# Performance work log

Hardware: AMD Instinct MI355X
Metric: run time of the kernel (lower is better)

## Reference

```python
import jax, jax.numpy as jnp
import numpy as np

DIM = 1024
HEADS = 8
DIM_HEAD = 64
INNER = HEADS * DIM_HEAD  # 512
LN_EPS = 1e-5


def setup_inputs() -> dict:
    key = jax.random.key(0)
    ks = jax.random.split(key, 8)
    b, n, m = 4, 2048, 512
    x = jax.random.normal(ks[0], (b, n, DIM), dtype=jnp.float32)
    media = jax.random.normal(ks[1], (b, m, DIM), dtype=jnp.float32)
    media_mask = jax.random.randint(ks[2], (b, m), 0, 2).astype(jnp.bool_)
    media_mask = media_mask.at[:, 0].set(True)  # avoid fully-masked rows
    ln_g = jnp.ones((DIM,), jnp.float32)
    ln_b = jnp.zeros((DIM,), jnp.float32)
    s = 0.02
    Wq = jax.random.normal(ks[3], (DIM, INNER), jnp.float32) * s
    Wkv = jax.random.normal(ks[4], (DIM, 2 * INNER), jnp.float32) * s
    Wo = jax.random.normal(ks[5], (INNER, DIM), jnp.float32) * s
    return {"x": x, "media": media, "media_mask": media_mask,
            "ln_g": ln_g, "ln_b": ln_b, "Wq": Wq, "Wkv": Wkv, "Wo": Wo}


def _layernorm(x, g, b):
    mu = jnp.mean(x, axis=-1, keepdims=True)
    var = jnp.var(x, axis=-1, keepdims=True)
    return (x - mu) * jax.lax.rsqrt(var + LN_EPS) * g + b


def reference(x, media, media_mask, ln_g, ln_b, Wq, Wkv, Wo):
    scale = DIM_HEAD ** (-0.5)
    xn = _layernorm(x, ln_g, ln_b)
    q = xn @ Wq                                  # (b, n, inner)
    kv = media @ Wkv                             # (b, m, 2*inner)
    k, v = jnp.split(kv, 2, axis=-1)
    # b n (h d) -> b h n d
    def split_heads(t):
        b_, s_, _ = t.shape
        return t.reshape(b_, s_, HEADS, DIM_HEAD).transpose(0, 2, 1, 3)
    q, k, v = split_heads(q) * scale, split_heads(k), split_heads(v)
    sim = jnp.einsum('bhid,bhjd->bhij', q, k)    # (b, h, n, m)
    neg_inf = jnp.finfo(sim.dtype).min
    sim = jnp.where(media_mask[:, None, None, :], sim, neg_inf)
    attn = jax.nn.softmax(sim, axis=-1)          # stable (max-subtract) softmax
    out = jnp.einsum('bhij,bhjd->bhid', attn, v)  # (b, h, n, d)
    out = out.transpose(0, 2, 1, 3).reshape(x.shape[0], x.shape[1], INNER)
    return out @ Wo
```

## Files before the change

### kernel.cpp

```cpp
#include <hip/hip_runtime.h>
#include <hip/hip_bf16.h>

typedef unsigned short u16;
typedef __attribute__((ext_vector_type(4))) unsigned short u16x4;
typedef __attribute__((ext_vector_type(8))) unsigned short u16x8;
typedef __attribute__((ext_vector_type(8))) short bf16x8;
typedef __attribute__((ext_vector_type(4))) float f32x4;

#define AS1 __attribute__((address_space(1)))
#define AS3 __attribute__((address_space(3)))

__device__ __forceinline__ float b2f(u16 v) {
    return __uint_as_float(((unsigned)v) << 16);
}
__device__ __forceinline__ u16 f2bf(float f) {
    unsigned u = __float_as_uint(f);
    unsigned r = (u + 0x7fffu + ((u >> 16) & 1u)) >> 16;
    return (u16)r;
}

__global__ __launch_bounds__(256) void prep_all(
    const float* __restrict__ x, const float* __restrict__ media,
    const unsigned char* __restrict__ mask,
    const float* __restrict__ ln_g, const float* __restrict__ ln_b,
    const float* __restrict__ Wq, const float* __restrict__ Wkv,
    const float* __restrict__ Wo,
    u16* __restrict__ xn, u16* __restrict__ mediab,
    unsigned char* __restrict__ mask8, int* __restrict__ idx,
    int* __restrict__ cnts,
    u16* __restrict__ wqt, u16* __restrict__ wkvt, u16* __restrict__ wot) {
    __shared__ u16 T[64][72];
    __shared__ int c0s, c1s;
    const int bid = blockIdx.x, tid = threadIdx.x;

    if (bid < 2048) {
        const int lane = tid & 63;
        const int row = bid * 4 + (tid >> 6);
        const float* xr = x + (size_t)row * 1024;
        float v[16];
        float sum = 0.f, sq = 0.f;
#pragma unroll
        for (int c = 0; c < 4; ++c) {
            float4 u = ((const float4*)xr)[c * 64 + lane];
            v[c * 4 + 0] = u.x; v[c * 4 + 1] = u.y; v[c * 4 + 2] = u.z; v[c * 4 + 3] = u.w;
            sum += u.x + u.y + u.z + u.w;
            sq += u.x * u.x + u.y * u.y + u.z * u.z + u.w * u.w;
        }
#pragma unroll
        for (int o = 1; o < 64; o <<= 1) {
            sum += __shfl_xor(sum, o, 64);
            sq += __shfl_xor(sq, o, 64);
        }
        float mean = sum * (1.f / 1024.f);
        float var = sq * (1.f / 1024.f) - mean * mean;
        float rs = rsqrtf(var + 1e-5f);
        u16* yr = xn + (size_t)row * 1024;
#pragma unroll
        for (int c = 0; c < 4; ++c) {
            float4 ug = ((const float4*)ln_g)[c * 64 + lane];
            float4 ub = ((const float4*)ln_b)[c * 64 + lane];
            u16x4 o;
            o[0] = f2bf((v[c * 4 + 0] - mean) * rs * ug.x + ub.x);
            o[1] = f2bf((v[c * 4 + 1] - mean) * rs * ug.y + ub.y);
            o[2] = f2bf((v[c * 4 + 2] - mean) * rs * ug.z + ub.z);
            o[3] = f2bf((v[c * 4 + 3] - mean) * rs * ug.w + ub.w);
            *(u16x4*)(yr + c * 256 + lane * 4) = o;
        }
    } else if (bid < 3072) {
        int i = (bid - 2048) * 256 + tid;
        float4 a = ((const float4*)media)[i * 2];
        float4 b = ((const float4*)media)[i * 2 + 1];
        u16x8 o;
        o[0] = f2bf(a.x); o[1] = f2bf(a.y); o[2] = f2bf(a.z); o[3] = f2bf(a.w);
        o[4] = f2bf(b.x); o[5] = f2bf(b.y); o[6] = f2bf(b.z); o[7] = f2bf(b.w);
        ((u16x8*)mediab)[i] = o;
    } else if (bid < 3840) {
        const int t = bid - 3072;
        const int z = t >> 8, rem = t & 255;
        const float* in; u16* out; int K, N;
        if (z == 0)      { in = Wq;  out = wqt;  K = 1024; N = 512; }
        else if (z == 1) { in = Wkv; out = wkvt; K = 1024; N = 1024; }
        else             { in = Wo;  out = wot;  K = 512;  N = 1024; }
        const int k0 = (rem >> 4) * 64, n0 = (rem & 15) * 64;
        if (k0 >= K || n0 >= N) return;
#pragma unroll
        for (int p = 0; p < 4; ++p) {
            int kr = p * 16 + (tid >> 4);
            float4 u = *(const float4*)(in + (size_t)(k0 + kr) * N + n0 + (tid & 15) * 4);
            u16x4 o4;
            o4[0] = f2bf(u.x); o4[1] = f2bf(u.y); o4[2] = f2bf(u.z); o4[3] = f2bf(u.w);
            *(u16x4*)(&T[kr][(tid & 15) * 4]) = o4;
        }
        __syncthreads();
        const int n = tid >> 2, kc = (tid & 3) * 16;
#pragma unroll
        for (int hh = 0; hh < 2; ++hh) {
            u16x8 o;
#pragma unroll
            for (int i = 0; i < 8; ++i) o[i] = T[kc + hh * 8 + i][n];
            *(u16x8*)(out + (size_t)(n0 + n) * K + k0 + kc + hh * 8) = o;
        }
    } else {
        if (tid == 0) { c0s = 0; c1s = 0; }
        __syncthreads();
        int a0 = 0, a1 = 0;
        for (int i = tid; i < 2048; i += 256) {
            if (mask[i]) {
                int cl = i & 3;
                if (cl == 0) a0 = 1;
                else if (cl == 1) a1 = 1;
            }
        }
        if (a0) atomicOr(&c0s, 1);
        if (a1) atomicOr(&c1s, 1);
        __syncthreads();
        int fmt = c1s ? 1 : (c0s ? 0 : 2);
        for (int e = tid; e < 2048; e += 256) {
            unsigned char v;
            if (fmt == 1)      v = (mask[e] != 0);
            else if (fmt == 0) v = (((const int*)mask)[e] != 0);
            else               v = (((const float*)mask)[e] != 0.f);
            mask8[e] = v;
        }
        __syncthreads();
        const int wv = tid >> 6, l = tid & 63;
        int off = 0;
#pragma unroll
        for (int c = 0; c < 8; ++c) {
            int key = c * 64 + l;
            bool v = mask8[wv * 512 + key] != 0;
            unsigned long long m = __ballot(v);
            int rank = __popcll(m & ((1ull << l) - 1ull));
            if (v) idx[wv * 512 + off + rank] = key;
            off += __popcll(m);
        }
        if (l == 0) cnts[wv] = off;
        int nt = (off + 127) & ~127;
        for (int p = off + l; p < nt; p += 64) idx[wv * 512 + p] = 0;
    }
}

template <int OUTF32, int GATHER>
__device__ __forceinline__ void gemm_tile_g(u16* As, u16* Bs,
                                            const u16* __restrict__ A,
                                            const u16* __restrict__ Bt,
                                            void* __restrict__ Cv,
                                            int N, int K, int row0, int col0,
                                            float scale,
                                            const int* __restrict__ ridx) {
    const int tid = threadIdx.x;
    const int l = tid & 63, w = tid >> 6;
    const int l15 = l & 15, l4 = l >> 4;
    const int wm = w >> 1, wn = w & 1;
    const int lr = l >> 3;
    const int cs = ((l & 7) ^ lr) * 8;

    int arow[4];
#pragma unroll
    for (int i = 0; i < 4; ++i) {
        int g = w * 32 + i * 8 + lr;
        arow[i] = GATHER ? ridx[row0 + g] : (row0 + g);
    }

    f32x4 zero = {0.f, 0.f, 0.f, 0.f};
    f32x4 acc[4][4];
#pragma unroll
    for (int i = 0; i < 4; ++i)
#pragma unroll
        for (int j = 0; j < 4; ++j) acc[i][j] = zero;

    const int rsw = l15 & 7;

    for (int k0 = 0; k0 < K; k0 += 64) {
        __syncthreads();
#pragma unroll
        for (int i = 0; i < 4; ++i) {
            int r = w * 32 + i * 8;
            __builtin_amdgcn_global_load_lds(
                (const AS1 void*)(A + (size_t)arow[i] * K + k0 + cs),
                (AS3 void*)(As + r * 64), 16, 0, 0);
            __builtin_amdgcn_global_load_lds(
                (const AS1 void*)(Bt + (size_t)(col0 + r + lr) * K + k0 + cs),
                (AS3 void*)(Bs + r * 64), 16, 0, 0);
        }
        __syncthreads();
#pragma unroll
        for (int h = 0; h < 2; ++h) {
            bf16x8 aF[4], bF[4];
#pragma unroll
            for (int m = 0; m < 4; ++m) {
                int s = (h * 4 + l4) ^ rsw;
                aF[m] = *(const bf16x8*)(As + (wm * 64 + m * 16 + l15) * 64 + s * 8);
                bF[m] = *(const bf16x8*)(Bs + (wn * 64 + m * 16 + l15) * 64 + s * 8);
            }
#pragma unroll
            for (int m = 0; m < 4; ++m)
#pragma unroll
                for (int n = 0; n < 4; ++n)
                    acc[m][n] = __builtin_amdgcn_mfma_f32_16x16x32_bf16(aF[m], bF[n], acc[m][n], 0, 0, 0);
        }
    }
#pragma unroll
    for (int m = 0; m < 4; ++m)
#pragma unroll
        for (int n = 0; n < 4; ++n) {
            int row = row0 + wm * 64 + m * 16 + l4 * 4;
            int col = col0 + wn * 64 + n * 16 + l15;
#pragma unroll
            for (int r = 0; r < 4; ++r) {
                float vv = acc[m][n][r] * scale;
                if (OUTF32)
                    ((float*)Cv)[(size_t)(row + r) * N + col] = vv;
                else
                    ((u16*)Cv)[(size_t)(row + r) * N + col] = f2bf(vv);
            }
        }
}

__global__ __launch_bounds__(256, 2) void qkv_gemm(const u16* __restrict__ xn,
                                                   const u16* __restrict__ wqt,
                                                   u16* __restrict__ qb,
                                                   const u16* __restrict__ mediab,
                                                   const u16* __restrict__ wkvt,
                                                   u16* __restrict__ kvb,
                                                   const int* __restrict__ idx,
                                                   const int* __restrict__ cnts) {
    __shared__ u16 As[128 * 64];
    __shared__ u16 Bs[128 * 64];
    const int b = blockIdx.x;
    if (b < 256) {
        gemm_tile_g<0, 0>(As, Bs, xn, wqt, (void*)qb, 512, 1024,
                          (b >> 2) * 128, (b & 3) * 128, 0.125f, nullptr);
    } else {
        const int t = b - 256;
        const int bbi = t >> 5, rem = t & 31;
        const int row0 = (rem >> 3) * 128, col0 = (rem & 7) * 128;
        const int nt128 = (cnts[bbi] + 127) & ~127;
        if (row0 >= nt128) return;
        gemm_tile_g<0, 1>(As, Bs, mediab + (size_t)bbi * 512 * 1024, wkvt,
                          (void*)(kvb + (size_t)bbi * 512 * 1024), 1024, 1024,
                          row0, col0, 1.f, idx + bbi * 512);
    }
}

__global__ __launch_bounds__(256, 2) void o_gemm(const u16* __restrict__ ao,
                                                 const u16* __restrict__ wot,
                                                 float* __restrict__ out) {
    __shared__ u16 As[128 * 64];
    __shared__ u16 Bs[128 * 64];
    gemm_tile_g<1, 0>(As, Bs, ao, wot, (void*)out, 1024, 512,
                      (int)blockIdx.y * 128, (int)blockIdx.x * 128, 1.f, nullptr);
}

__global__ __launch_bounds__(256) void attn_mfma(const u16* __restrict__ qb,
                                                 const u16* __restrict__ kvb,
                                                 const int* __restrict__ cnts,
                                                 u16* __restrict__ ao) {
    __shared__ u16 Ks[64][72];
    __shared__ u16 Vt[64][72];
    __shared__ u16 Pl[4][16][72];
    const int tid = threadIdx.x;
    const int l = tid & 63, w = tid >> 6;
    const int l15 = l & 15, l4 = l >> 4;
    const int h = blockIdx.y, bbi = blockIdx.z;
    const int n0 = blockIdx.x * 64;
    const int cnt = cnts[bbi];

    const u16* qp = qb + ((size_t)(bbi * 2048 + n0 + w * 16 + l15)) * 512 + h * 64;
    const bf16x8 qf0 = *(const bf16x8*)(qp + l4 * 8);
    const bf16x8 qf1 = *(const bf16x8*)(qp + 32 + l4 * 8);

    const f32x4 zero = {0.f, 0.f, 0.f, 0.f};
    f32x4 acc[4];
#pragma unroll
    for (int dt = 0; dt < 4; ++dt) acc[dt] = zero;
    float mrun[4] = {-3.0e38f, -3.0e38f, -3.0e38f, -3.0e38f};
    float lrun[4] = {0.f, 0.f, 0.f, 0.f};

    const int kj = tid >> 3, kd = (tid & 7) * 8;
    const int vj = tid & 63, vd = (tid >> 6) * 16;
    const u16* kbase = kvb + ((size_t)bbi * 512) * 1024 + h * 64;

    for (int j0 = 0; j0 < cnt; j0 += 64) {
        __syncthreads();
#pragma unroll
        for (int p = 0; p < 2; ++p) {
            int r = kj + p * 32;
            u16x8 kv_ = *(const u16x8*)(kbase + (size_t)(j0 + r) * 1024 + kd);
            *(u16x8*)(&Ks[r][kd]) = kv_;
        }
        {
#pragma unroll
            for (int p = 0; p < 2; ++p) {
                u16x8 vv = *(const u16x8*)(kbase + (size_t)(j0 + vj) * 1024 + 512 + vd + p * 8);
#pragma unroll
                for (int i = 0; i < 8; ++i) Vt[vd + p * 8 + i][vj] = vv[i];
            }
        }
        __syncthreads();

        f32x4 s[4];
        float mv[4];
#pragma unroll
        for (int jt = 0; jt < 4; ++jt) {
            bf16x8 kf0 = *(const bf16x8*)(&Ks[jt * 16 + l15][l4 * 8]);
            bf16x8 kf1 = *(const bf16x8*)(&Ks[jt * 16 + l15][32 + l4 * 8]);
            s[jt] = __builtin_amdgcn_mfma_f32_16x16x32_bf16(qf0, kf0, zero, 0, 0, 0);
            s[jt] = __builtin_amdgcn_mfma_f32_16x16x32_bf16(qf1, kf1, s[jt], 0, 0, 0);
            mv[jt] = (j0 + jt * 16 + l15 < cnt) ? 0.f : -3.0e38f;
        }

        float sv[4][4];
        float pmax[4];
        bool cond = true;
#pragma unroll
        for (int r = 0; r < 4; ++r) {
#pragma unroll
            for (int jt = 0; jt < 4; ++jt) sv[r][jt] = s[jt][r] + mv[jt];
            pmax[r] = fmaxf(fmaxf(sv[r][0], sv[r][1]), fmaxf(sv[r][2], sv[r][3]));
            cond = cond && (pmax[r] <= mrun[r] + 8.f);
        }
        if (__all(cond)) {
#pragma unroll
            for (int r = 0; r < 4; ++r) {
                float p0 = __expf(sv[r][0] - mrun[r]);
                float p1 = __expf(sv[r][1] - mrun[r]);
                float p2 = __expf(sv[r][2] - mrun[r]);
                float p3 = __expf(sv[r][3] - mrun[r]);
                lrun[r] += (p0 + p1) + (p2 + p3);
                Pl[w][l4 * 4 + r][l15] = f2bf(p0);
                Pl[w][l4 * 4 + r][16 + l15] = f2bf(p1);
                Pl[w][l4 * 4 + r][32 + l15] = f2bf(p2);
                Pl[w][l4 * 4 + r][48 + l15] = f2bf(p3);
            }
        } else {
#pragma unroll
            for (int r = 0; r < 4; ++r) {
                float tmax = pmax[r];
#pragma unroll
                for (int o = 1; o < 16; o <<= 1) tmax = fmaxf(tmax, __shfl_xor(tmax, o, 64));
                float mn = fmaxf(mrun[r], tmax);
                float corr = __expf(mrun[r] - mn);
                mrun[r] = mn;
                float p0 = __expf(sv[r][0] - mn);
                float p1 = __expf(sv[r][1] - mn);
                float p2 = __expf(sv[r][2] - mn);
                float p3 = __expf(sv[r][3] - mn);
                lrun[r] = lrun[r] * corr + (p0 + p1) + (p2 + p3);
#pragma unroll
                for (int dt = 0; dt < 4; ++dt) acc[dt][r] *= corr;
                Pl[w][l4 * 4 + r][l15] = f2bf(p0);
                Pl[w][l4 * 4 + r][16 + l15] = f2bf(p1);
                Pl[w][l4 * 4 + r][32 + l15] = f2bf(p2);
                Pl[w][l4 * 4 + r][48 + l15] = f2bf(p3);
            }
        }
        bf16x8 pf0 = *(const bf16x8*)(&Pl[w][l15][l4 * 8]);
        bf16x8 pf1 = *(const bf16x8*)(&Pl[w][l15][32 + l4 * 8]);
#pragma unroll
        for (int dt = 0; dt < 4; ++dt) {
            bf16x8 vf0 = *(const bf16x8*)(&Vt[dt * 16 + l15][l4 * 8]);
            bf16x8 vf1 = *(const bf16x8*)(&Vt[dt * 16 + l15][32 + l4 * 8]);
            acc[dt] = __builtin_amdgcn_mfma_f32_16x16x32_bf16(pf0, vf0, acc[dt], 0, 0, 0);
            acc[dt] = __builtin_amdgcn_mfma_f32_16x16x32_bf16(pf1, vf1, acc[dt], 0, 0, 0);
        }
    }

    float inv[4];
#pragma unroll
    for (int r = 0; r < 4; ++r) {
        float lt = lrun[r];
#pragma unroll
        for (int o = 1; o < 16; o <<= 1) lt += __shfl_xor(lt, o, 64);
        inv[r] = (lt > 0.f) ? (1.f / lt) : 0.f;
    }
    u16* op = ao + ((size_t)(bbi * 2048 + n0 + w * 16)) * 512 + h * 64;
#pragma unroll
    for (int dt = 0; dt < 4; ++dt)
#pragma unroll
        for (int r = 0; r < 4; ++r)
            op[(size_t)(l4 * 4 + r) * 512 + dt * 16 + l15] = f2bf(acc[dt][r] * inv[r]);
}

extern "C" void kernel_launch(void* const* d_in, const int* in_sizes, int n_in,
                              void* d_out, int out_size, void* d_ws, size_t ws_size,
                              hipStream_t stream) {
    const float* x = (const float*)d_in[0];
    const float* media = (const float*)d_in[1];
    const unsigned char* mask = (const unsigned char*)d_in[2];
    const float* ln_g = (const float*)d_in[3];
    const float* ln_b = (const float*)d_in[4];
    const float* Wq = (const float*)d_in[5];
    const float* Wkv = (const float*)d_in[6];
    const float* Wo = (const float*)d_in[7];
    float* out = (float*)d_out;

    char* w = (char*)d_ws;
    unsigned char* mask8 = (unsigned char*)w; w += 4096;
    int* idx = (int*)w;    w += 2048 * 4;
    int* cnts = (int*)w;   w += 256;
    u16* qb = (u16*)w;     w += (size_t)8192 * 512 * 2;
    u16* kvb = (u16*)w;    w += (size_t)2048 * 1024 * 2;
    u16* ao = (u16*)w;     w += (size_t)8192 * 512 * 2;
    u16* mediab = (u16*)w; w += (size_t)2048 * 1024 * 2;
    u16* wqt = (u16*)w;    w += (size_t)512 * 1024 * 2;
    u16* wkvt = (u16*)w;   w += (size_t)1024 * 1024 * 2;
    u16* wot = (u16*)w;    w += (size_t)1024 * 512 * 2;
    u16* xn = (u16*)d_out;

    prep_all<<<3841, 256, 0, stream>>>(x, media, mask, ln_g, ln_b, Wq, Wkv, Wo,
                                       xn, mediab, mask8, idx, cnts, wqt, wkvt, wot);
    qkv_gemm<<<384, 256, 0, stream>>>(xn, wqt, qb, mediab, wkvt, kvb, idx, cnts);
    attn_mfma<<<dim3(32, 8, 4), 256, 0, stream>>>(qb, kvb, cnts, ao);
    o_gemm<<<dim3(8, 64), 256, 0, stream>>>(ao, wot, out);
}
```

Baseline: 76.57 us.

## Double-buffer LDS tiles in GEMM with async prefetch of next K tile

```diff
diff --git a/kernel.cpp b/kernel.cpp
--- a/kernel.cpp
+++ b/kernel.cpp
@@ -170,28 +170,50 @@
         for (int j = 0; j < 4; ++j) acc[i][j] = zero;
 
     const int rsw = l15 & 7;
-
-    for (int k0 = 0; k0 < K; k0 += 64) {
-        __syncthreads();
-#pragma unroll
-        for (int i = 0; i < 4; ++i) {
-            int r = w * 32 + i * 8;
-            __builtin_amdgcn_global_load_lds(
-                (const AS1 void*)(A + (size_t)arow[i] * K + k0 + cs),
-                (AS3 void*)(As + r * 64), 16, 0, 0);
-            __builtin_amdgcn_global_load_lds(
-                (const AS1 void*)(Bt + (size_t)(col0 + r + lr) * K + k0 + cs),
-                (AS3 void*)(Bs + r * 64), 16, 0, 0);
-        }
-        __syncthreads();
+    const int nt = K >> 6;
+
+#pragma unroll
+    for (int i = 0; i < 4; ++i) {
+        int r = w * 32 + i * 8;
+        __builtin_amdgcn_global_load_lds(
+            (const AS1 void*)(A + (size_t)arow[i] * K + cs),
+            (AS3 void*)(As + r * 64), 16, 0, 0);
+        __builtin_amdgcn_global_load_lds(
+            (const AS1 void*)(Bt + (size_t)(col0 + r + lr) * K + cs),
+            (AS3 void*)(Bs + r * 64), 16, 0, 0);
+    }
+
+    for (int t = 0; t < nt; ++t) {
+        const int cur = (t & 1) * (128 * 64);
+        if (t + 1 < nt) {
+            const int nxt = ((t + 1) & 1) * (128 * 64);
+            const int k1 = (t + 1) << 6;
+#pragma unroll
+            for (int i = 0; i < 4; ++i) {
+                int r = w * 32 + i * 8;
+                __builtin_amdgcn_global_load_lds(
+                    (const AS1 void*)(A + (size_t)arow[i] * K + k1 + cs),
+                    (AS3 void*)(As + nxt + r * 64), 16, 0, 0);
+                __builtin_amdgcn_global_load_lds(
+                    (const AS1 void*)(Bt + (size_t)(col0 + r + lr) * K + k1 + cs),
+                    (AS3 void*)(Bs + nxt + r * 64), 16, 0, 0);
+            }
+            asm volatile("s_waitcnt vmcnt(8)");
+        } else {
+            asm volatile("s_waitcnt vmcnt(0)");
+        }
+        __builtin_amdgcn_sched_barrier(0);
+        __builtin_amdgcn_s_barrier();
+        __builtin_amdgcn_sched_barrier(0);
+
 #pragma unroll
         for (int h = 0; h < 2; ++h) {
             bf16x8 aF[4], bF[4];
 #pragma unroll
             for (int m = 0; m < 4; ++m) {
                 int s = (h * 4 + l4) ^ rsw;
-                aF[m] = *(const bf16x8*)(As + (wm * 64 + m * 16 + l15) * 64 + s * 8);
-                bF[m] = *(const bf16x8*)(Bs + (wn * 64 + m * 16 + l15) * 64 + s * 8);
+                aF[m] = *(const bf16x8*)(As + cur + (wm * 64 + m * 16 + l15) * 64 + s * 8);
+                bF[m] = *(const bf16x8*)(Bs + cur + (wn * 64 + m * 16 + l15) * 64 + s * 8);
             }
 #pragma unroll
             for (int m = 0; m < 4; ++m)
@@ -199,6 +221,7 @@
                 for (int n = 0; n < 4; ++n)
                     acc[m][n] = __builtin_amdgcn_mfma_f32_16x16x32_bf16(aF[m], bF[n], acc[m][n], 0, 0, 0);
         }
+        __builtin_amdgcn_s_barrier();
     }
 #pragma unroll
     for (int m = 0; m < 4; ++m)
@@ -225,8 +248,8 @@
                                                    u16* __restrict__ kvb,
                                                    const int* __restrict__ idx,
                                                    const int* __restrict__ cnts) {
-    __shared__ u16 As[128 * 64];
-    __shared__ u16 Bs[128 * 64];
+    __shared__ u16 As[2 * 128 * 64];
+    __shared__ u16 Bs[2 * 128 * 64];
     const int b = blockIdx.x;
     if (b < 256) {
         gemm_tile_g<0, 0>(As, Bs, xn, wqt, (void*)qb, 512, 1024,
@@ -246,8 +269,8 @@
 __global__ __launch_bounds__(256, 2) void o_gemm(const u16* __restrict__ ao,
                                                  const u16* __restrict__ wot,
                                                  float* __restrict__ out) {
-    __shared__ u16 As[128 * 64];
-    __shared__ u16 Bs[128 * 64];
+    __shared__ u16 As[2 * 128 * 64];
+    __shared__ u16 Bs[2 * 128 * 64];
     gemm_tile_g<1, 0>(As, Bs, ao, wot, (void*)out, 1024, 512,
                       (int)blockIdx.y * 128, (int)blockIdx.x * 128, 1.f, nullptr);
 }
```

Measured after the change: 76.26 us. No clear change (-0.4%).
